# Performance work log

Hardware: AMD Instinct MI355X
Metric: run time of the kernel (lower is better)

## Reference

```python
import jax, jax.numpy as jnp
import numpy as np


def _local_linear(x, W, b=None):
    # Faithful to Local_Linear: split last dim into G groups, apply per-group
    # Linear, then stack groups on the LAST axis and flatten -> output channel
    # index is o*G + g (interleaved), NOT block-diagonal order.
    B, N, C = x.shape
    G, og, ig = W.shape
    y = jnp.einsum('bngi,goi->bngo', x.reshape(B, N, G, ig), W)  # [B,N,G,og]
    if b is not None:
        y = y + b
    return jnp.swapaxes(y, -1, -2).reshape(B, N, G * og)  # [B,N,og,G] -> flat


def setup_inputs() -> dict:
    key = jax.random.key(0)
    ks = jax.random.split(key, 6)
    B, N, dim, H = 16, 8192, 128, 2
    hd = dim // H
    s = 1.0 / np.sqrt(hd).astype(np.float32)
    return {
        'x': jax.random.normal(ks[0], (B, N, dim), jnp.float32),
        'Wk': jax.random.normal(ks[1], (H, hd, hd), jnp.float32) * s,
        'Wv': jax.random.normal(ks[2], (H, hd, hd), jnp.float32) * s,
        'Wp': jax.random.normal(ks[3], (H, hd, hd), jnp.float32) * s,
        'bp': jax.random.normal(ks[4], (H, hd), jnp.float32) * 0.01,
        'mem': jax.random.normal(ks[5], (H, hd), jnp.float32) * 0.02,
    }


def reference(x, Wk, Wv, Wp, bp, mem):
    B, N, C = x.shape
    H, hd = mem.shape
    scale = hd ** -0.5
    # k, v: [B, H, N, hd] (view of interleaved grouped-linear output, as in torch)
    k = _local_linear(x, Wk).reshape(B, N, H, hd).transpose(0, 2, 1, 3)
    v = _local_linear(x, Wv).reshape(B, N, H, hd).transpose(0, 2, 1, 3)
    # The query (memory_bank) is identical for every position, so the [N,N]
    # attention matrix has identical rows -> compute one row per (b,h).
    s = jnp.einsum('hd,bhmd->bhm', mem, k) * scale          # logits over keys
    a = jax.nn.softmax(s, axis=-1)                          # [B,H,N]
    row = jnp.einsum('bhm,bhmd->bhd', a, v)                 # [B,H,hd]
    # torch does out.view(B,N,-1) WITHOUT permuting heads back; [B,H,N,hd]
    # reshaped directly to [B,N,C]. Replicate that exact layout.
    out = jnp.broadcast_to(row[:, :, None, :], (B, H, N, hd)).reshape(B, N, C)
    return _local_linear(out, Wp, bp)
```

## Files before the change

kernel.cpp:

```cpp
#include <hip/hip_runtime.h>
#include <hip/hip_bf16.h>

#define B_      16
#define N_      8192
#define C_      128
#define HD_     64
#define TILE_N  64
#define NBLK    (N_ / TILE_N)
#define OTIL    64
#define PART_STRIDE 260

typedef float v4f __attribute__((ext_vector_type(4)));


__global__ __launch_bounds__(256) void k_partial(
    const float* __restrict__ x,
    const float* __restrict__ Wk,
    const float* __restrict__ mem,
    float* __restrict__ part)
{
    __shared__ float qeff0[C_], qeff1[C_];
    __shared__ float sp0[4][TILE_N], sp1[4][TILE_N];
    __shared__ float sl0[TILE_N], sl1[TILE_N];
    __shared__ float paf0[8][C_], paf1[8][C_];
    __shared__ float redm[2];

    const int t   = threadIdx.x;
    const int blk = blockIdx.x;
    const int b   = blk >> 7;
    const int tl  = blk & 127;
    const int n0  = tl * TILE_N;

    {
        const int h = t >> 7, c = t & 127, g = c >> 6, i = c & 63;
        const float* wkb = Wk + g * 4096 + (h * 32) * 64 + i;
        const float* mr  = mem + h * 64 + g;
        float a = 0.f;
        #pragma unroll
        for (int j = 0; j < 32; ++j) a += mr[2 * j] * wkb[j * 64];
        if (h == 0) qeff0[c] = 0.125f * a; else qeff1[c] = 0.125f * a;
    }
    __syncthreads();

    {
        const int r = t & 63, q4 = t >> 6;
        const float4* xr = (const float4*)(x + ((size_t)b * N_ + n0 + r) * C_ + q4 * 32);
        float p0 = 0.f, p1 = 0.f;
        #pragma unroll
        for (int v = 0; v < 8; ++v) {
            const float4 q = xr[v];
            const int c0 = q4 * 32 + v * 4;
            p0 += q.x * qeff0[c0]     + q.y * qeff0[c0 + 1]
                + q.z * qeff0[c0 + 2] + q.w * qeff0[c0 + 3];
            p1 += q.x * qeff1[c0]     + q.y * qeff1[c0 + 1]
                + q.z * qeff1[c0 + 2] + q.w * qeff1[c0 + 3];
        }
        sp0[q4][r] = p0;
        sp1[q4][r] = p1;
    }
    __syncthreads();

    if (t < TILE_N) {
        const float s0 = sp0[0][t] + sp0[1][t] + sp0[2][t] + sp0[3][t];
        const float s1 = sp1[0][t] + sp1[1][t] + sp1[2][t] + sp1[3][t];
        float w0 = __expf(s0);
        float w1 = __expf(s1);
        sl0[t] = w0;
        sl1[t] = w1;
        float l0 = w0, l1 = w1;
        #pragma unroll
        for (int off = 32; off > 0; off >>= 1) {
            l0 += __shfl_xor(l0, off);
            l1 += __shfl_xor(l1, off);
        }
        if (t == 0) { redm[0] = l0; redm[1] = l1; }
    }
    __syncthreads();

    {
        const int c4 = t & 31, rg = t >> 5;
        const float* xg = x + ((size_t)b * N_ + n0 + rg * 8) * C_ + c4 * 4;
        v4f a0 = {0.f, 0.f, 0.f, 0.f};
        v4f a1 = {0.f, 0.f, 0.f, 0.f};
        #pragma unroll
        for (int k = 0; k < 8; ++k) {
            const v4f q = *(const v4f*)(xg + (size_t)k * C_);
            const float w0r = sl0[rg * 8 + k];
            const float w1r = sl1[rg * 8 + k];
            a0.x += w0r * q.x; a0.y += w0r * q.y; a0.z += w0r * q.z; a0.w += w0r * q.w;
            a1.x += w1r * q.x; a1.y += w1r * q.y; a1.z += w1r * q.z; a1.w += w1r * q.w;
        }
        *(v4f*)&paf0[rg][c4 * 4] = a0;
        *(v4f*)&paf1[rg][c4 * 4] = a1;
    }
    __syncthreads();

    float* p = part + (size_t)blk * PART_STRIDE;
    if (t < C_) {
        float s0a = 0.f, s1a = 0.f;
        #pragma unroll
        for (int g = 0; g < 8; ++g) { s0a += paf0[g][t]; s1a += paf1[g][t]; }
        p[4 + t]       = s0a;
        p[4 + C_ + t]  = s1a;
    }
    if (t == 0) {
        p[0] = redm[0];
        p[1] = redm[1];
    }
}

__global__ __launch_bounds__(256) void k_fused(
    const float* __restrict__ part,
    const float* __restrict__ Wv,
    const float* __restrict__ Wp,
    const float* __restrict__ bp,
    v4f* __restrict__ out4)
{
    __shared__ float paf[8][C_];
    __shared__ float redl[2];
    __shared__ float xan[C_];
    __shared__ float rowv[HD_];
    __shared__ float Ff[C_];

    const int t   = threadIdx.x;
    const int blk = blockIdx.x;
    const int b   = blk >> 6;
    const int tl  = blk & 63;
    const int h   = tl >> 5;

    const float* pb = part + (size_t)b * NBLK * PART_STRIDE;

    if (t < NBLK) {
        float lv = pb[(size_t)t * PART_STRIDE + h];
        #pragma unroll
        for (int off = 32; off > 0; off >>= 1) lv += __shfl_xor(lv, off);
        if ((t & 63) == 0) redl[t >> 6] = lv;
    }

    {
        const int c4 = t & 31, kg = t >> 5;
        const float* qb = pb + (size_t)(kg * 16) * PART_STRIDE + 4 + h * C_ + c4 * 4;
        v4f a = {0.f, 0.f, 0.f, 0.f};
        #pragma unroll
        for (int k = 0; k < 16; ++k) {
            const v4f q = *(const v4f*)(qb + (size_t)k * PART_STRIDE);
            a.x += q.x; a.y += q.y; a.z += q.z; a.w += q.w;
        }
        *(v4f*)&paf[kg][c4 * 4] = a;
    }
    __syncthreads();
    if (t < C_) {
        float s = 0.f;
        #pragma unroll
        for (int g = 0; g < 8; ++g) s += paf[g][t];
        xan[t] = s / (redl[0] + redl[1]);
    }
    __syncthreads();

    if (t < HD_) {
        const int g = t & 1, o = h * 32 + (t >> 1);
        const v4f* wv4 = (const v4f*)(Wv + g * 4096 + o * 64);
        const v4f* xv4 = (const v4f*)&xan[g * 64];
        v4f a4 = {0.f, 0.f, 0.f, 0.f};
        #pragma unroll
        for (int i = 0; i < 16; ++i) {
            const v4f wq = wv4[i], xq = xv4[i];
            a4.x += wq.x * xq.x; a4.y += wq.y * xq.y;
            a4.z += wq.z * xq.z; a4.w += wq.w * xq.w;
        }
        rowv[t] = a4.x + a4.y + a4.z + a4.w;
    }
    __syncthreads();

    if (t < C_) {
        const int g = t & 1, o = t >> 1;
        const v4f* wp4 = (const v4f*)(Wp + g * 4096 + o * 64);
        const v4f* rv4 = (const v4f*)rowv;
        v4f a4 = {0.f, 0.f, 0.f, 0.f};
        #pragma unroll
        for (int i = 0; i < 16; ++i) {
            const v4f wq = wp4[i], rq = rv4[i];
            a4.x += wq.x * rq.x; a4.y += wq.y * rq.y;
            a4.z += wq.z * rq.z; a4.w += wq.w * rq.w;
        }
        Ff[t] = bp[g * 64 + o] + a4.x + a4.y + a4.z + a4.w;
    }
    __syncthreads();

    const v4f val = *(const v4f*)&Ff[(t & 31) * 4];
    v4f* dst = out4 + (size_t)b * (N_ * (C_ / 4)) + (size_t)tl * (128 * (C_ / 4)) + t;
    #pragma unroll
    for (int k = 0; k < 16; ++k)
        __builtin_nontemporal_store(val, dst + k * 256);
}

extern "C" void kernel_launch(void* const* d_in, const int* in_sizes, int n_in,
                              void* d_out, int out_size, void* d_ws, size_t ws_size,
                              hipStream_t stream)
{
    const float* x   = (const float*)d_in[0];
    const float* Wk  = (const float*)d_in[1];
    const float* Wv  = (const float*)d_in[2];
    const float* Wp  = (const float*)d_in[3];
    const float* bp  = (const float*)d_in[4];
    const float* mem = (const float*)d_in[5];

    float* part = (float*)d_ws;

    k_partial<<<dim3(B_ * NBLK), dim3(256), 0, stream>>>(x, Wk, mem, part);
    k_fused<<<dim3(B_ * OTIL), dim3(256), 0, stream>>>(part, Wv, Wp, bp,
                                                       (v4f*)d_out);
}
```

Baseline: 133.9 us.

## Load x tile into registers once and reuse for logits and weighted sum

k_partial now loads each thread's slice of the x tile into registers at kernel start, before the query projection, and reuses those registers for both the logit dot products and the exp-weighted accumulation. Before, the tile was read from global memory twice. Logit partials are written to a padded shared buffer and reduced per row by 128 threads. The shared buffer is also reused for the final column reduction, which all 256 threads now perform. This removes the second global read of x and lets the load overlap the qeff computation, at the cost of more registers and a longer serial per-row reduction.

Result: faster. 127.3 us (median of 2 runs) (-4.9%).

```diff
diff --git a/kernel.cpp b/kernel.cpp
--- a/kernel.cpp
+++ b/kernel.cpp
@@ -19,10 +19,9 @@
     const float* __restrict__ mem,
     float* __restrict__ part)
 {
-    __shared__ float qeff0[C_], qeff1[C_];
-    __shared__ float sp0[4][TILE_N], sp1[4][TILE_N];
-    __shared__ float sl0[TILE_N], sl1[TILE_N];
-    __shared__ float paf0[8][C_], paf1[8][C_];
+    __shared__ __align__(16) float qeff0[C_], qeff1[C_];
+    __shared__ __align__(16) float ubuf[2 * 64 * 33];
+    __shared__ float wsh[2][TILE_N];
     __shared__ float redm[2];
 
     const int t   = threadIdx.x;
@@ -30,6 +29,16 @@
     const int b   = blk >> 7;
     const int tl  = blk & 127;
     const int n0  = tl * TILE_N;
+    const int c4  = t & 31;
+    const int rg  = t >> 5;
+
+    v4f q[8];
+    {
+        const float* xb = x + ((size_t)b * N_ + n0 + rg) * C_ + 4 * c4;
+        #pragma unroll
+        for (int v = 0; v < 8; ++v)
+            q[v] = *(const v4f*)(xb + (size_t)(8 * v) * C_);
+    }
 
     {
         const int h = t >> 7, c = t & 127, g = c >> 6, i = c & 63;
@@ -43,65 +52,59 @@
     __syncthreads();
 
     {
-        const int r = t & 63, q4 = t >> 6;
-        const float4* xr = (const float4*)(x + ((size_t)b * N_ + n0 + r) * C_ + q4 * 32);
-        float p0 = 0.f, p1 = 0.f;
+        const v4f e0 = *(const v4f*)&qeff0[4 * c4];
+        const v4f e1 = *(const v4f*)&qeff1[4 * c4];
         #pragma unroll
         for (int v = 0; v < 8; ++v) {
-            const float4 q = xr[v];
-            const int c0 = q4 * 32 + v * 4;
-            p0 += q.x * qeff0[c0]     + q.y * qeff0[c0 + 1]
-                + q.z * qeff0[c0 + 2] + q.w * qeff0[c0 + 3];
-            p1 += q.x * qeff1[c0]     + q.y * qeff1[c0 + 1]
-                + q.z * qeff1[c0 + 2] + q.w * qeff1[c0 + 3];
-        }
-        sp0[q4][r] = p0;
-        sp1[q4][r] = p1;
-    }
-    __syncthreads();
-
-    if (t < TILE_N) {
-        const float s0 = sp0[0][t] + sp0[1][t] + sp0[2][t] + sp0[3][t];
-        const float s1 = sp1[0][t] + sp1[1][t] + sp1[2][t] + sp1[3][t];
-        float w0 = __expf(s0);
-        float w1 = __expf(s1);
-        sl0[t] = w0;
-        sl1[t] = w1;
-        float l0 = w0, l1 = w1;
-        #pragma unroll
-        for (int off = 32; off > 0; off >>= 1) {
-            l0 += __shfl_xor(l0, off);
-            l1 += __shfl_xor(l1, off);
-        }
-        if (t == 0) { redm[0] = l0; redm[1] = l1; }
-    }
-    __syncthreads();
-
-    {
-        const int c4 = t & 31, rg = t >> 5;
-        const float* xg = x + ((size_t)b * N_ + n0 + rg * 8) * C_ + c4 * 4;
+            const int rw = 8 * v + rg;
+            ubuf[(0 * 64 + rw) * 33 + c4] =
+                q[v].x * e0.x + q[v].y * e0.y + q[v].z * e0.z + q[v].w * e0.w;
+            ubuf[(1 * 64 + rw) * 33 + c4] =
+                q[v].x * e1.x + q[v].y * e1.y + q[v].z * e1.z + q[v].w * e1.w;
+        }
+    }
+    __syncthreads();
+
+    if (t < 128) {
+        const int h = t >> 6, r = t & 63;
+        const float* sr = &ubuf[(h * 64 + r) * 33];
+        float s = 0.f;
+        #pragma unroll
+        for (int k = 0; k < 32; ++k) s += sr[k];
+        const float w = __expf(s);
+        wsh[h][r] = w;
+        float l = w;
+        #pragma unroll
+        for (int off = 32; off > 0; off >>= 1) l += __shfl_xor(l, off);
+        if (r == 0) redm[h] = l;
+    }
+    __syncthreads();
+
+    {
         v4f a0 = {0.f, 0.f, 0.f, 0.f};
         v4f a1 = {0.f, 0.f, 0.f, 0.f};
         #pragma unroll
-        for (int k = 0; k < 8; ++k) {
-            const v4f q = *(const v4f*)(xg + (size_t)k * C_);
-            const float w0r = sl0[rg * 8 + k];
-            const float w1r = sl1[rg * 8 + k];
-            a0.x += w0r * q.x; a0.y += w0r * q.y; a0.z += w0r * q.z; a0.w += w0r * q.w;
-            a1.x += w1r * q.x; a1.y += w1r * q.y; a1.z += w1r * q.z; a1.w += w1r * q.w;
-        }
-        *(v4f*)&paf0[rg][c4 * 4] = a0;
-        *(v4f*)&paf1[rg][c4 * 4] = a1;
+        for (int v = 0; v < 8; ++v) {
+            const int rw = 8 * v + rg;
+            const float w0 = wsh[0][rw];
+            const float w1 = wsh[1][rw];
+            a0.x += w0 * q[v].x; a0.y += w0 * q[v].y;
+            a0.z += w0 * q[v].z; a0.w += w0 * q[v].w;
+            a1.x += w1 * q[v].x; a1.y += w1 * q[v].y;
+            a1.z += w1 * q[v].z; a1.w += w1 * q[v].w;
+        }
+        *(v4f*)&ubuf[(0 * 8 + rg) * 132 + 4 * c4] = a0;
+        *(v4f*)&ubuf[(1 * 8 + rg) * 132 + 4 * c4] = a1;
     }
     __syncthreads();
 
     float* p = part + (size_t)blk * PART_STRIDE;
-    if (t < C_) {
-        float s0a = 0.f, s1a = 0.f;
-        #pragma unroll
-        for (int g = 0; g < 8; ++g) { s0a += paf0[g][t]; s1a += paf1[g][t]; }
-        p[4 + t]       = s0a;
-        p[4 + C_ + t]  = s1a;
+    {
+        const int h = t >> 7, c = t & 127;
+        float s = 0.f;
+        #pragma unroll
+        for (int g = 0; g < 8; ++g) s += ubuf[(h * 8 + g) * 132 + c];
+        p[4 + h * C_ + c] = s;
     }
     if (t == 0) {
         p[0] = redm[0];
```
